# Kernel optimization log

Hardware: AMD Instinct MI355X
Metric: run time of the kernel (lower is better)

The kernel has to match this reference:

```python
import jax, jax.numpy as jnp
import numpy as np

D = 1024   # model dim (hard-coded in ClsNet)
H = 16     # num_heads
HD = D // H
FF = 2048  # torch TransformerEncoderLayer default dim_feedforward
B, LX, LY = 8, 512, 512
EPS = 1e-5
NEG = -1e9


def setup_inputs() -> dict:
    key = jax.random.key(0)
    ks = jax.random.split(key, 16)
    s = 0.02
    inp = {
        "x": jax.random.normal(ks[0], (B, LX, D), jnp.float32),
        "y": jax.random.normal(ks[1], (B, LY, D), jnp.float32),
        "cls": jax.random.normal(ks[2], (D,), jnp.float32) * s,
        "sep": jax.random.normal(ks[3], (D,), jnp.float32) * s,
        "px": jax.random.normal(ks[4], (D,), jnp.float32) * s,
        "py": jax.random.normal(ks[5], (D,), jnp.float32) * s,
        "Wqkv": jax.random.normal(ks[6], (3 * D, D), jnp.float32) * s,
        "bqkv": jnp.zeros((3 * D,), jnp.float32),
        "Wo": jax.random.normal(ks[7], (D, D), jnp.float32) * s,
        "bo": jnp.zeros((D,), jnp.float32),
        "W1": jax.random.normal(ks[8], (FF, D), jnp.float32) * s,
        "b1": jnp.zeros((FF,), jnp.float32),
        "W2": jax.random.normal(ks[9], (D, FF), jnp.float32) * s,
        "b2": jnp.zeros((D,), jnp.float32),
        "ln1_g": jnp.ones((D,), jnp.float32),
        "ln1_b": jnp.zeros((D,), jnp.float32),
        "ln2_g": jnp.ones((D,), jnp.float32),
        "ln2_b": jnp.zeros((D,), jnp.float32),
        "x_len": jax.random.randint(ks[10], (B,), 1, LX + 1, jnp.int32),
        "y_len": jax.random.randint(ks[11], (B,), 1, LY + 1, jnp.int32),
    }
    return inp


def _merge(x, y, cls, sep, px, py, x_len, y_len):
    # Vectorized version of ClsNet.merge: [CLS] x_i+px ... [SEP] y_i+py ... [SEP] pad...
    Bn, Lx, Dd = x.shape
    Ly = y.shape[1]
    S = Lx + Ly + 3
    pos = jnp.arange(S)[None, :]            # [1,S]
    lx = x_len[:, None]                     # [B,1]
    ly = y_len[:, None]
    is_cls = pos == 0                       # [1,S]
    is_x = (pos >= 1) & (pos <= lx)         # [B,S]
    is_sep1 = pos == lx + 1
    is_y = (pos >= lx + 2) & (pos <= lx + ly + 1)
    is_sep2 = pos == lx + ly + 2
    xi = jnp.clip(pos - 1, 0, Lx - 1)       # [1,S]
    yi = jnp.clip(pos - lx - 2, 0, Ly - 1)  # [B,S]
    xg = jnp.take_along_axis(x, xi[:, :, None], axis=1)  # [B,S,D] (broadcast batch)
    yg = jnp.take_along_axis(y, yi[:, :, None], axis=1)  # [B,S,D]
    seq = (jnp.where(is_x[..., None], xg + px, 0.0)
           + jnp.where(is_y[..., None], yg + py, 0.0)
           + is_cls[..., None] * cls
           + (is_sep1 | is_sep2)[..., None] * sep)       # [B,S,D]
    mask = is_cls | is_x | is_sep1 | is_y | is_sep2      # [B,S] True = valid token
    return seq, mask


def _ln(h, g, b):
    m = jnp.mean(h, axis=-1, keepdims=True)
    v = jnp.mean(jnp.square(h - m), axis=-1, keepdims=True)
    return (h - m) * jax.lax.rsqrt(v + EPS) * g + b


def _encoder_layer(seq, mask, Wqkv, bqkv, Wo, bo, W1, b1, W2, b2, ln1_g, ln1_b, ln2_g, ln2_b):
    Bn, S, Dd = seq.shape
    qkv = seq @ Wqkv.T + bqkv                              # [B,S,3D]
    q, k, v = jnp.split(qkv, 3, axis=-1)
    q = q.reshape(Bn, S, H, HD)
    k = k.reshape(Bn, S, H, HD)
    v = v.reshape(Bn, S, H, HD)
    bias = jnp.where(mask, 0.0, NEG)[:, None, None, :]     # padded KEYS masked out
    scores = jnp.einsum("bqhd,bkhd->bhqk", q, k) / np.sqrt(HD) + bias
    attn = jax.nn.softmax(scores, axis=-1)
    o = jnp.einsum("bhqk,bkhd->bqhd", attn, v).reshape(Bn, S, Dd)
    o = o @ Wo.T + bo
    h = _ln(seq + o, ln1_g, ln1_b)                          # post-norm (torch default)
    f = jax.nn.relu(h @ W1.T + b1) @ W2.T + b2
    return _ln(h + f, ln2_g, ln2_b)


def reference(x, y, cls, sep, px, py, Wqkv, bqkv, Wo, bo, W1, b1, W2, b2,
              ln1_g, ln1_b, ln2_g, ln2_b, x_len, y_len):
    seq, mask = _merge(x, y, cls, sep, px, py, x_len, y_len)
    out = _encoder_layer(seq, mask, Wqkv, bqkv, Wo, bo, W1, b1, W2, b2,
                         ln1_g, ln1_b, ln2_g, ln2_b)
    # torch code returns a[0] of the seq-first tensor -> the CLS position for all batches
    return out[:, 0, :]
```

## Files before the change

### kernel.cpp

```cpp
#include <hip/hip_runtime.h>
#include <hip/hip_bf16.h>

#define D_ 1024
#define H_ 16
#define FF_ 2048
#define B_ 8
#define S_ 1027
#define BS_ 8216
#define MPAD_ 8320
#define PSTR_ 1056
#define EPS_ 1e-5f
#define MAXGRID_ 512
#define NTILE_ 130

#define OFF_SEQ  0
#define OFF_RTHI 17039360
#define OFF_RTLO 17072128
#define OFF_S    17104896
#define OFF_P    17637376
#define OFF_CBAR 17907712
#define OFF_O0   20004864
#define OFF_ATT  20037632
#define OFF_F1   20070400
#define OFF_F2   20103168
#define OFF_BAR  20135936
#define OFF_Q0S  20140032
#define OFF_H0   20144128

typedef __hip_bfloat16 bf16;
typedef unsigned short u16;
typedef unsigned int u32;
typedef __attribute__((ext_vector_type(4))) float floatx4;
typedef __bf16 bf16x8 __attribute__((ext_vector_type(8)));

__device__ __forceinline__ float2 bfpair(u32 u) {
  union { u32 u; float f; } lo, hi;
  lo.u = u << 16; hi.u = u & 0xffff0000u;
  return make_float2(lo.f, hi.f);
}

__device__ __forceinline__ u32 f2bfbits(float f) {
  union { bf16 h; u16 u; } cv; cv.h = __float2bfloat16(f); return (u32)cv.u;
}

__device__ __forceinline__ void st_wt_f32(float* p, float v) {
  asm volatile("global_store_dword %0, %1, off sc0 sc1" :: "v"(p), "v"(v) : "memory");
}
__device__ __forceinline__ void st_wt_u16(u16* p, u32 v) {
  asm volatile("global_store_short %0, %1, off sc0 sc1" :: "v"(p), "v"(v) : "memory");
}
__device__ __forceinline__ void st_wt_v2(void* p, uint2 v) {
  asm volatile("global_store_dwordx2 %0, %1, off sc0 sc1" :: "v"(p), "v"(v) : "memory");
}
__device__ __forceinline__ void st_wt_f4(void* p, floatx4 v) {
  asm volatile("global_store_dwordx4 %0, %1, off sc0 sc1" :: "v"(p), "v"(v) : "memory");
}

__device__ __forceinline__ float blk_sum(float x, float* red) {
#pragma unroll
  for (int off = 32; off > 0; off >>= 1) x += __shfl_down(x, off, 64);
  __syncthreads();
  if ((threadIdx.x & 63) == 0) red[threadIdx.x >> 6] = x;
  __syncthreads();
  return red[0] + red[1] + red[2] + red[3];
}

__device__ __forceinline__ float blk_max(float x, float* red) {
#pragma unroll
  for (int off = 32; off > 0; off >>= 1) x = fmaxf(x, __shfl_down(x, off, 64));
  __syncthreads();
  if ((threadIdx.x & 63) == 0) red[threadIdx.x >> 6] = x;
  __syncthreads();
  return fmaxf(fmaxf(red[0], red[1]), fmaxf(red[2], red[3]));
}

__device__ __forceinline__ void gridbar(u32* bar, u32 phase) {
  asm volatile("s_waitcnt vmcnt(0) lgkmcnt(0)" ::: "memory");
  __syncthreads();
  if (threadIdx.x == 0) {
    __hip_atomic_fetch_add(bar + (blockIdx.x & 7) * 16, 1u,
                           __ATOMIC_RELAXED, __HIP_MEMORY_SCOPE_AGENT);
    const u32 target = (u32)gridDim.x * phase;
    int spins = 0;
    for (;;) {
      u32 s = 0;
#pragma unroll
      for (int i = 0; i < 8; ++i)
        s += __hip_atomic_load(bar + i * 16, __ATOMIC_RELAXED,
                               __HIP_MEMORY_SCOPE_AGENT);
      if (s >= target) break;
      __builtin_amdgcn_s_sleep(2);
      if (++spins > 400000) break;
    }
  }
  __syncthreads();
}

struct KP {
  const float *x, *y, *cls, *sep, *px, *py;
  const float *Wqkv, *bqkv, *Wo, *bo, *W1, *b1, *W2, *b2;
  const float *g1, *be1, *g2, *be2;
  const int *xl, *yl;
  bf16* seq; u16* RT_hi; u16* RT_lo; float* S; u16* P;
  float* cbar; float* o0; float* att; bf16* f1; float* f2; float* out;
  u32* bar;
};

__device__ __forceinline__ const float* row_src(const KP& p, int m,
                                                const int* lx8, const int* ly8,
                                                const float** add) {
  const int b = m / S_;
  const int s = m - b * S_;
  const int lx = lx8[b], ly = ly8[b];
  *add = nullptr;
  if (s == 0) return p.cls;
  if (s <= lx) { *add = p.px; return p.x + ((size_t)b * 512 + (s - 1)) * D_; }
  if (s == lx + 1) return p.sep;
  if (s <= lx + ly + 1) { *add = p.py; return p.y + ((size_t)b * 512 + (s - lx - 2)) * D_; }
  if (s == lx + ly + 2) return p.sep;
  return nullptr;
}

__global__ void __launch_bounds__(256, 2) mega_kernel(KP p) {
  __shared__ __align__(16) char smem_[33792];
  const int t = threadIdx.x;
  const int bid = blockIdx.x;
  const int G = gridDim.x;

  if (t == 0) __builtin_amdgcn_fence(__ATOMIC_ACQUIRE, "agent");
  __syncthreads();

  if (bid < 64) {
    const int h = bid >> 2, cc = bid & 3;
    float* cl = (float*)smem_;
    float* qs = (float*)(smem_ + 4096);
    *(float4*)&cl[t * 4] = ((const float4*)p.cls)[t];
    __syncthreads();
    const int r = t >> 2, j = t & 3;
    const float* wr = p.Wqkv + (size_t)(h * 64 + r) * D_;
    float acc = 0.f;
#pragma unroll 8
    for (int i = 0; i < 64; ++i) {
      float4 wv = *(const float4*)(wr + i * 16 + j * 4);
      const float* c4 = &cl[i * 16 + j * 4];
      acc += wv.x * c4[0] + wv.y * c4[1] + wv.z * c4[2] + wv.w * c4[3];
    }
    acc += __shfl_xor(acc, 1, 64);
    acc += __shfl_xor(acc, 2, 64);
    if (j == 0) qs[r] = (acc + p.bqkv[h * 64 + r]) * 0.125f;
    __syncthreads();
    const int c = cc * 256 + t;
    const float* Wk = p.Wqkv + (size_t)(D_ + h * 64) * D_ + c;
    float a2 = 0.f;
#pragma unroll 8
    for (int e = 0; e < 64; ++e) a2 += Wk[(size_t)e * D_] * qs[e];
    const u32 hb = f2bfbits(a2);
    union { u32 u; float f; } hv; hv.u = hb << 16;
    st_wt_u16(p.RT_hi + h * D_ + c, hb);
    st_wt_u16(p.RT_lo + h * D_ + c, f2bfbits(a2 - hv.f));
  } else {
    int lx8[8], ly8[8];
#pragma unroll
    for (int b = 0; b < 8; ++b) { lx8[b] = p.xl[b]; ly8[b] = p.yl[b]; }
    const int stride = G - 64;
    for (int m0 = bid - 64; m0 < BS_; m0 += 2 * stride) {
      const int m1 = m0 + stride;
      const float *ad0, *ad1 = nullptr;
      const float* s0 = row_src(p, m0, lx8, ly8, &ad0);
      const float* s1 = (m1 < BS_) ? row_src(p, m1, lx8, ly8, &ad1) : nullptr;
      float4 v0, a0v, v1, a1v;
      if (s0) v0 = ((const float4*)s0)[t];
      if (ad0) a0v = ((const float4*)ad0)[t];
      if (s1) v1 = ((const float4*)s1)[t];
      if (ad1) a1v = ((const float4*)ad1)[t];
      if (s0) {
        if (ad0) { v0.x += a0v.x; v0.y += a0v.y; v0.z += a0v.z; v0.w += a0v.w; }
        uint2 o;
        o.x = f2bfbits(v0.x) | (f2bfbits(v0.y) << 16);
        o.y = f2bfbits(v0.z) | (f2bfbits(v0.w) << 16);
        st_wt_v2((u16*)p.seq + (size_t)m0 * D_ + t * 4, o);
      }
      if (s1) {
        if (ad1) { v1.x += a1v.x; v1.y += a1v.y; v1.z += a1v.z; v1.w += a1v.w; }
        uint2 o;
        o.x = f2bfbits(v1.x) | (f2bfbits(v1.y) << 16);
        o.y = f2bfbits(v1.z) | (f2bfbits(v1.w) << 16);
        st_wt_v2((u16*)p.seq + (size_t)m1 * D_ + t * 4, o);
      }
    }
  }
  gridbar(p.bar, 1);

  for (int wk = bid; wk < NTILE_; wk += G) {
    const int m0 = wk * 64;
    bool valid = false;
#pragma unroll
    for (int b = 0; b < B_; ++b) {
      int rs = b * S_, re = rs + p.xl[b] + p.yl[b] + 3;
      if (m0 < re && m0 + 64 > rs) valid = true;
    }
    if (!valid) continue;
    const int w = t >> 6, lane = t & 63, lane16 = lane & 15, quad = lane >> 4;
    const int row = m0 + w * 16 + lane16;
    const u16* arow = (const u16*)p.seq + (size_t)row * D_ + quad * 8;
    const u16* bh = p.RT_hi + lane16 * D_ + quad * 8;
    const u16* bl = p.RT_lo + lane16 * D_ + quad * 8;
    floatx4 acc = {};
#pragma unroll 4
    for (int kt = 0; kt < 32; ++kt) {
      bf16x8 a  = *(const bf16x8*)(arow + kt * 32);
      bf16x8 vh = *(const bf16x8*)(bh + kt * 32);
      bf16x8 vl = *(const bf16x8*)(bl + kt * 32);
      acc = __builtin_amdgcn_mfma_f32_16x16x32_bf16(a, vh, acc, 0, 0, 0);
      acc = __builtin_amdgcn_mfma_f32_16x16x32_bf16(a, vl, acc, 0, 0, 0);
    }
    st_wt_f4(&p.S[(size_t)lane16 * MPAD_ + m0 + w * 16 + quad * 4], acc);
  }
  gridbar(p.bar, 2);

  {
    floatx4 z = {};
    for (int idx = bid * 256 + t; idx < 32768; idx += G * 256)
      st_wt_f4(p.cbar + (size_t)idx * 4, z);
  }
  for (int wk = bid; wk < 128; wk += G) {
    const int h = wk >> 3, b = wk & 7;
    const int n = p.xl[b] + p.yl[b] + 3;
    float* sc = (float*)smem_;
    float* red = (float*)(smem_ + PSTR_ * 4);
    const float* Sp = p.S + (size_t)h * MPAD_ + b * S_;
    float lmax = -3.0e38f;
    for (int k = t; k < n; k += 256) {
      float s = Sp[k];
      sc[k] = s;
      lmax = fmaxf(lmax, s);
    }
    const float gmax = blk_max(lmax, red);
    float lsum = 0.f;
    for (int k = t; k < n; k += 256) {
      float pr = __expf(sc[k] - gmax);
      sc[k] = pr;
      lsum += pr;
    }
    const float inv = 1.0f / blk_sum(lsum, red);
    u16* Pp = p.P + (size_t)(h * 8 + b) * PSTR_;
    for (int k = t; k < PSTR_; k += 256)
      st_wt_u16(Pp + k, (k < n) ? f2bfbits(sc[k] * inv) : 0u);
    __syncthreads();
  }
  gridbar(p.bar, 3);

  for (int wk = bid; wk < 512; wk += G) {
    const int ct = wk & 15, b = (wk >> 4) & 7, piece = wk >> 7;
    const int c0 = ct * 64;
    const int n = p.xl[b] + p.yl[b] + 3;
    const int nkt = (n + 31) >> 5;
    const int KR0[4] = {0, 9, 17, 25};
    const int KR1[4] = {9, 17, 25, 33};
    const int kt0 = KR0[piece];
    const int kt1 = nkt < KR1[piece] ? nkt : KR1[piece];
    u16* tile = (u16*)smem_;
    const int w = t >> 6, lane = t & 63, lane16 = lane & 15, quad = lane >> 4;
    const int sk = t >> 3, scg = (t & 7) * 8;
    floatx4 acc = {};
    uint4 v = make_uint4(0u, 0u, 0u, 0u);
    if (kt0 < kt1 && kt0 * 32 + sk < n)
      v = *(const uint4*)((const u16*)p.seq + (size_t)((size_t)b * S_ + kt0 * 32 + sk) * D_ + c0 + scg);
    bool any = (kt0 < kt1);
    for (int kt = kt0; kt < kt1; ++kt) {
      u16* tb = tile + (kt & 1) * (32 * 68);
      *(uint2*)&tb[sk * 68 + scg]     = make_uint2(v.x, v.y);
      *(uint2*)&tb[sk * 68 + scg + 4] = make_uint2(v.z, v.w);
      v = make_uint4(0u, 0u, 0u, 0u);
      if (kt + 1 < kt1 && (kt + 1) * 32 + sk < n)
        v = *(const uint4*)((const u16*)p.seq + (size_t)((size_t)b * S_ + (kt + 1) * 32 + sk) * D_ + c0 + scg);
      __syncthreads();
      bf16x8 a = *(const bf16x8*)(p.P + (size_t)(lane16 * 8 + b) * PSTR_ + kt * 32 + quad * 8);
      union { bf16x8 v8; u16 u[8]; } bu;
#pragma unroll
      for (int j = 0; j < 8; ++j)
        bu.u[j] = tb[(quad * 8 + j) * 68 + w * 16 + lane16];
      acc = __builtin_amdgcn_mfma_f32_16x16x32_bf16(a, bu.v8, acc, 0, 0, 0);
    }
    if (any) {
#pragma unroll
      for (int r = 0; r < 4; ++r)
        atomicAdd(&p.cbar[(size_t)(b * 16 + quad * 4 + r) * D_ + c0 + w * 16 + lane16], acc[r]);
    }
    __syncthreads();
  }
  gridbar(p.bar, 4);

  for (int wk = bid; wk < 256; wk += G) {
    float* lsf = (float*)smem_;
    const int hoff = ((wk * 4) >> 6) * D_;
#pragma unroll
    for (int i = 0; i < 8; ++i) {
      int flat = (t + i * 256) * 4;
      int b = flat >> 10, k = flat & 1023;
      *(float4*)&lsf[flat] = *(const float4*)(p.cbar + (size_t)b * 16384 + hoff + k);
    }
    __syncthreads();
    const int w = t >> 6, l = t & 63;
    const int r = wk * 4 + w;
    const float* W = p.Wqkv + (size_t)2048 * 1024;
    float acc[8] = {};
#pragma unroll
    for (int ch = 0; ch < 4; ++ch) {
      float4 wv = *(const float4*)(W + (size_t)r * D_ + ch * 256 + l * 4);
#pragma unroll
      for (int b = 0; b < 8; ++b) {
        const float* pp = &lsf[b * D_ + ch * 256 + l * 4];
        acc[b] += wv.x * pp[0] + wv.y * pp[1] + wv.z * pp[2] + wv.w * pp[3];
      }
    }
#pragma unroll
    for (int off = 32; off > 0; off >>= 1)
#pragma unroll
      for (int b = 0; b < 8; ++b) acc[b] += __shfl_down(acc[b], off, 64);
    if (l == 0) {
      const float bs = p.bqkv[2048 + r];
#pragma unroll
      for (int b = 0; b < 8; ++b) st_wt_f32(&p.o0[(size_t)b * D_ + r], acc[b] + bs);
    }
    __syncthreads();
  }
  gridbar(p.bar, 5);

  for (int wk = bid; wk < 256; wk += G) {
    float* lsf = (float*)smem_;
#pragma unroll
    for (int i = 0; i < 8; ++i) {
      int flat = (t + i * 256) * 4;
      *(float4*)&lsf[flat] = *(const float4*)(p.o0 + flat);
    }
    __syncthreads();
    const int w = t >> 6, l = t & 63;
    const int r = wk * 4 + w;
    float acc[8] = {};
#pragma unroll
    for (int ch = 0; ch < 4; ++ch) {
      float4 wv = *(const float4*)(p.Wo + (size_t)r * D_ + ch * 256 + l * 4);
#pragma unroll
      for (int b = 0; b < 8; ++b) {
        const float* pp = &lsf[b * D_ + ch * 256 + l * 4];
        acc[b] += wv.x * pp[0] + wv.y * pp[1] + wv.z * pp[2] + wv.w * pp[3];
      }
    }
#pragma unroll
    for (int off = 32; off > 0; off >>= 1)
#pragma unroll
      for (int b = 0; b < 8; ++b) acc[b] += __shfl_down(acc[b], off, 64);
    if (l == 0) {
      const float bs = p.bo[r];
#pragma unroll
      for (int b = 0; b < 8; ++b) st_wt_f32(&p.att[(size_t)b * D_ + r], acc[b] + bs);
    }
    __syncthreads();
  }
  gridbar(p.bar, 6);

  for (int wk = bid; wk < 512; wk += G) {
    float* lsf = (float*)smem_;
#pragma unroll
    for (int i = 0; i < 8; ++i) {
      int flat = (t + i * 256) * 4;
      int b = flat >> 10, k = flat & 1023;
      float4 av = *(const float4*)(p.att + (size_t)b * D_ + k);
      float4 cv = *(const float4*)(p.cls + k);
      av.x += cv.x; av.y += cv.y; av.z += cv.z; av.w += cv.w;
      *(float4*)&lsf[flat] = av;
    }
    __syncthreads();
    const int w = t >> 6, l = t & 63;
#pragma unroll
    for (int bb = 2 * w; bb < 2 * w + 2; ++bb) {
      float s = 0.f;
#pragma unroll
      for (int kk = 0; kk < 16; ++kk) s += lsf[bb * 1024 + kk * 64 + l];
#pragma unroll
      for (int off = 32; off > 0; off >>= 1) s += __shfl_xor(s, off, 64);
      const float mean = s * (1.f / D_);
      float vv = 0.f;
#pragma unroll
      for (int kk = 0; kk < 16; ++kk) {
        float d = lsf[bb * 1024 + kk * 64 + l] - mean; vv += d * d;
      }
#pragma unroll
      for (int off = 32; off > 0; off >>= 1) vv += __shfl_xor(vv, off, 64);
      const float rs = rsqrtf(vv * (1.f / D_) + EPS_);
#pragma unroll
      for (int kk = 0; kk < 16; ++kk) {
        int idx = kk * 64 + l;
        lsf[bb * 1024 + idx] =
            (lsf[bb * 1024 + idx] - mean) * rs * p.g1[idx] + p.be1[idx];
      }
    }
    __syncthreads();
    const int r = wk * 4 + w;
    float acc[8] = {};
#pragma unroll
    for (int ch = 0; ch < 4; ++ch) {
      float4 wv = *(const float4*)(p.W1 + (size_t)r * D_ + ch * 256 + l * 4);
#pragma unroll
      for (int b = 0; b < 8; ++b) {
        const float* pp = &lsf[b * D_ + ch * 256 + l * 4];
        acc[b] += wv.x * pp[0] + wv.y * pp[1] + wv.z * pp[2] + wv.w * pp[3];
      }
    }
#pragma unroll
    for (int off = 32; off > 0; off >>= 1)
#pragma unroll
      for (int b = 0; b < 8; ++b) acc[b] += __shfl_down(acc[b], off, 64);
    if (l == 0) {
      const float bs = p.b1[r];
#pragma unroll
      for (int b = 0; b < 8; ++b)
        st_wt_u16((u16*)p.f1 + (size_t)b * FF_ + r, f2bfbits(fmaxf(acc[b] + bs, 0.f)));
    }
    __syncthreads();
  }
  gridbar(p.bar, 7);

  for (int wk = bid; wk < 256; wk += G) {
    u16* lsb = (u16*)smem_;
#pragma unroll
    for (int i = 0; i < 8; ++i) {
      int flat = (t + i * 256) * 8;
      *(uint4*)&lsb[flat] = *(const uint4*)((const u16*)p.f1 + flat);
    }
    __syncthreads();
    const int w = t >> 6, l = t & 63;
    const int r = wk * 4 + w;
    float acc[8] = {};
#pragma unroll
    for (int ch = 0; ch < 8; ++ch) {
      float4 wv = *(const float4*)(p.W2 + (size_t)r * FF_ + ch * 256 + l * 4);
#pragma unroll
      for (int b = 0; b < 8; ++b) {
        uint2 u = *(const uint2*)&lsb[b * FF_ + ch * 256 + l * 4];
        float2 p0 = bfpair(u.x), p1 = bfpair(u.y);
        acc[b] += wv.x * p0.x + wv.y * p0.y + wv.z * p1.x + wv.w * p1.y;
      }
    }
#pragma unroll
    for (int off = 32; off > 0; off >>= 1)
#pragma unroll
      for (int b = 0; b < 8; ++b) acc[b] += __shfl_down(acc[b], off, 64);
    if (l == 0) {
      const float bs = p.b2[r];
#pragma unroll
      for (int b = 0; b < 8; ++b) st_wt_f32(&p.f2[(size_t)b * D_ + r], acc[b] + bs);
    }
    __syncthreads();
  }
  gridbar(p.bar, 8);

  for (int wk = bid; wk < 8; wk += G) {
    float* v = (float*)smem_;
    float* red = (float*)(smem_ + D_ * 4);
    for (int i = t; i < D_; i += 256) v[i] = p.cls[i] + p.att[wk * D_ + i];
    __syncthreads();
    float ls = 0.f;
    for (int i = t; i < D_; i += 256) ls += v[i];
    const float mean1 = blk_sum(ls, red) * (1.f / D_);
    float lv = 0.f;
    for (int i = t; i < D_; i += 256) { float dk = v[i] - mean1; lv += dk * dk; }
    const float var1 = blk_sum(lv, red) * (1.f / D_);
    const float rs1 = rsqrtf(var1 + EPS_);
    for (int i = t; i < D_; i += 256) {
      float h0v = (v[i] - mean1) * rs1 * p.g1[i] + p.be1[i];
      v[i] = h0v + p.f2[wk * D_ + i];
    }
    __syncthreads();
    float ls2 = 0.f;
    for (int i = t; i < D_; i += 256) ls2 += v[i];
    const float mean2 = blk_sum(ls2, red) * (1.f / D_);
    float lv2 = 0.f;
    for (int i = t; i < D_; i += 256) { float dk = v[i] - mean2; lv2 += dk * dk; }
    const float var2 = blk_sum(lv2, red) * (1.f / D_);
    const float rs2 = rsqrtf(var2 + EPS_);
    for (int i = t; i < D_; i += 256)
      p.out[wk * D_ + i] = (v[i] - mean2) * rs2 * p.g2[i] + p.be2[i];
    __syncthreads();
  }
}

__device__ __forceinline__ float block_sum(float x, float* red) {
  const int t = threadIdx.x;
  __syncthreads();
  red[t] = x;
  __syncthreads();
  for (int s = 128; s > 0; s >>= 1) {
    if (t < s) red[t] += red[t + s];
    __syncthreads();
  }
  return red[0];
}

__device__ __forceinline__ float block_max(float x, float* red) {
  const int t = threadIdx.x;
  __syncthreads();
  red[t] = x;
  __syncthreads();
  for (int s = 128; s > 0; s >>= 1) {
    if (t < s) red[t] = fmaxf(red[t], red[t + s]);
    __syncthreads();
  }
  return red[0];
}

__global__ void __launch_bounds__(256) build_seq_kernel(
    const float* __restrict__ x, const float* __restrict__ y,
    const float* __restrict__ cls, const float* __restrict__ sep,
    const float* __restrict__ px, const float* __restrict__ py,
    const int* __restrict__ x_len, const int* __restrict__ y_len,
    bf16* __restrict__ seq) {
  const int m = blockIdx.x, t = threadIdx.x;
  const int b = m / S_;
  const int s = m - b * S_;
  if (b >= B_) return;
  const float* src = nullptr;
  const float* add = nullptr;
  const int lx = x_len[b], ly = y_len[b];
  if (s == 0) src = cls;
  else if (s <= lx) { src = x + ((size_t)b * 512 + (s - 1)) * D_; add = px; }
  else if (s == lx + 1) src = sep;
  else if (s <= lx + ly + 1) { src = y + ((size_t)b * 512 + (s - lx - 2)) * D_; add = py; }
  else if (s == lx + ly + 2) src = sep;
  if (!src) return;
  float4 sv = ((const float4*)src)[t];
  if (add) {
    float4 av = ((const float4*)add)[t];
    sv.x += av.x; sv.y += av.y; sv.z += av.z; sv.w += av.w;
  }
  uint2 o;
  o.x = f2bfbits(sv.x) | (f2bfbits(sv.y) << 16);
  o.y = f2bfbits(sv.z) | (f2bfbits(sv.w) << 16);
  ((uint2*)(seq + (size_t)m * D_))[t] = o;
}

__global__ void __launch_bounds__(256) qproj_kernel(
    const float* __restrict__ cls, const float* __restrict__ Wqkv,
    const float* __restrict__ bqkv, float* __restrict__ q0s) {
  __shared__ float cl[D_];
  const int t = threadIdx.x;
  *(float4*)&cl[t * 4] = ((const float4*)cls)[t];
  __syncthreads();
  const int w = t >> 6, l = t & 63;
  const int r = blockIdx.x * 4 + w;
  float acc = 0.f;
#pragma unroll
  for (int ch = 0; ch < 4; ++ch) {
    float4 wv = *(const float4*)(Wqkv + (size_t)r * D_ + ch * 256 + l * 4);
    const float* c4 = &cl[ch * 256 + l * 4];
    acc += wv.x * c4[0] + wv.y * c4[1] + wv.z * c4[2] + wv.w * c4[3];
  }
#pragma unroll
  for (int off = 32; off > 0; off >>= 1) acc += __shfl_down(acc, off, 64);
  if (l == 0) q0s[r] = (acc + bqkv[r]) * 0.125f;
}

__global__ void __launch_bounds__(256) rproj_kernel(
    const float* __restrict__ Wqkv, const float* __restrict__ q0s,
    u16* __restrict__ RT_hi, u16* __restrict__ RT_lo) {
  const int h = blockIdx.y, cc = blockIdx.x, t = threadIdx.x;
  __shared__ float qs[64];
  if (t < 64) qs[t] = q0s[h * 64 + t];
  __syncthreads();
  const int c = cc * 256 + t;
  const float* Wk = Wqkv + (size_t)(D_ + h * 64) * D_ + c;
  float acc = 0.f;
#pragma unroll 8
  for (int e = 0; e < 64; ++e) acc += Wk[(size_t)e * D_] * qs[e];
  const u32 hb = f2bfbits(acc);
  union { u32 u; float f; } hv; hv.u = hb << 16;
  RT_hi[h * D_ + c] = (u16)hb;
  RT_lo[h * D_ + c] = (u16)f2bfbits(acc - hv.f);
}

__global__ void __launch_bounds__(256) scores_kernel(
    const bf16* __restrict__ seq, const u16* __restrict__ RT_hi,
    const u16* __restrict__ RT_lo, const int* __restrict__ x_len,
    const int* __restrict__ y_len, float* __restrict__ S) {
  const int m0 = blockIdx.x * 64;
  bool valid = false;
#pragma unroll
  for (int b = 0; b < B_; ++b) {
    int rs = b * S_, re = rs + x_len[b] + y_len[b] + 3;
    if (m0 < re && m0 + 64 > rs) valid = true;
  }
  if (!valid) return;
  const int t = threadIdx.x;
  const int w = t >> 6, lane = t & 63, lane16 = lane & 15, quad = lane >> 4;
  const int row = m0 + w * 16 + lane16;
  const u16* arow = (const u16*)seq + (size_t)row * D_ + quad * 8;
  const u16* bh = RT_hi + lane16 * D_ + quad * 8;
  const u16* bl = RT_lo + lane16 * D_ + quad * 8;
  floatx4 acc = {};
#pragma unroll 4
  for (int kt = 0; kt < 32; ++kt) {
    bf16x8 a  = *(const bf16x8*)(arow + kt * 32);
    bf16x8 vh = *(const bf16x8*)(bh + kt * 32);
    bf16x8 vl = *(const bf16x8*)(bl + kt * 32);
    acc = __builtin_amdgcn_mfma_f32_16x16x32_bf16(a, vh, acc, 0, 0, 0);
    acc = __builtin_amdgcn_mfma_f32_16x16x32_bf16(a, vl, acc, 0, 0, 0);
  }
  *(floatx4*)&S[(size_t)lane16 * MPAD_ + m0 + w * 16 + quad * 4] = acc;
}

__global__ void __launch_bounds__(256) softmax_kernel(
    const float* __restrict__ S, const int* __restrict__ x_len,
    const int* __restrict__ y_len, u16* __restrict__ P) {
  const int h = blockIdx.x, b = blockIdx.y, t = threadIdx.x;
  const int n = x_len[b] + y_len[b] + 3;
  __shared__ float sc[PSTR_];
  __shared__ float red[256];
  const float* Sp = S + (size_t)h * MPAD_ + b * S_;
  float lmax = -3.0e38f;
  for (int k = t; k < n; k += 256) {
    float s = Sp[k];
    sc[k] = s;
    lmax = fmaxf(lmax, s);
  }
  const float gmax = block_max(lmax, red);
  float lsum = 0.f;
  for (int k = t; k < n; k += 256) {
    float p = __expf(sc[k] - gmax);
    sc[k] = p;
    lsum += p;
  }
  const float inv = 1.0f / block_sum(lsum, red);
  u16* Pp = P + (size_t)(h * 8 + b) * PSTR_;
  for (int k = t; k < PSTR_; k += 256)
    Pp[k] = (k < n) ? (u16)f2bfbits(sc[k] * inv) : (u16)0;
}

__global__ void __launch_bounds__(256) cbar_kernel(
    const bf16* __restrict__ seq, const u16* __restrict__ P,
    const int* __restrict__ x_len, const int* __restrict__ y_len,
    float* __restrict__ cbar) {
  const int ct = blockIdx.x, b = blockIdx.y, t = threadIdx.x;
  const int c0 = ct * 64;
  const int n = x_len[b] + y_len[b] + 3;
  const int nkt = (n + 31) >> 5;
  __shared__ u16 tile[32 * 68];
  const int w = t >> 6, lane = t & 63, lane16 = lane & 15, quad = lane >> 4;
  const int sk = t >> 3, scg = (t & 7) * 8;
  floatx4 acc = {};
  for (int kt = 0; kt < nkt; ++kt) {
    const int k0 = kt * 32;
    __syncthreads();
    uint4 v = make_uint4(0u, 0u, 0u, 0u);
    if (k0 + sk < n)
      v = *(const uint4*)((const u16*)seq + (size_t)(b * S_ + k0 + sk) * D_ + c0 + scg);
    *(uint2*)&tile[sk * 68 + scg]     = make_uint2(v.x, v.y);
    *(uint2*)&tile[sk * 68 + scg + 4] = make_uint2(v.z, v.w);
    __syncthreads();
    bf16x8 a = *(const bf16x8*)(P + (size_t)(lane16 * 8 + b) * PSTR_ + k0 + quad * 8);
    union { bf16x8 v; u16 u[8]; } bu;
#pragma unroll
    for (int j = 0; j < 8; ++j)
      bu.u[j] = tile[(quad * 8 + j) * 68 + w * 16 + lane16];
    acc = __builtin_amdgcn_mfma_f32_16x16x32_bf16(a, bu.v, acc, 0, 0, 0);
  }
#pragma unroll
  for (int r = 0; r < 4; ++r)
    cbar[(size_t)(b * 16 + quad * 4 + r) * D_ + c0 + w * 16 + lane16] = acc[r];
}

template <int K, int N, int BSTR, bool INBF, bool OUTBF, bool RELU, bool PERHEAD>
__global__ void __launch_bounds__(256) gemv8_kernel(
    const void* __restrict__ in_, const float* __restrict__ W,
    const float* __restrict__ bias, void* __restrict__ out_) {
  const int t = threadIdx.x;
  const int hoff = PERHEAD ? ((blockIdx.x * 4) >> 6) * D_ : 0;
  __shared__ u16 lsb[INBF ? 8 * K : 1];
  __shared__ float lsf[INBF ? 1 : 8 * K];
  if (INBF) {
    const u16* in = (const u16*)in_;
    const int per = 8 * K / (256 * 8);
#pragma unroll
    for (int i = 0; i < per; ++i) {
      int flat = (t + i * 256) * 8;
      int b = flat / K, k = flat % K;
      *(uint4*)&lsb[flat] = *(const uint4*)(in + (size_t)b * BSTR + hoff + k);
    }
  } else {
    const float* in = (const float*)in_;
    const int per = 8 * K / (256 * 4);
#pragma unroll
    for (int i = 0; i < per; ++i) {
      int flat = (t + i * 256) * 4;
      int b = flat / K, k = flat % K;
      *(float4*)&lsf[flat] = *(const float4*)(in + (size_t)b * BSTR + hoff + k);
    }
  }
  __syncthreads();
  const int w = t >> 6, l = t & 63;
  const int r = blockIdx.x * 4 + w;
  float acc[8] = {};
#pragma unroll
  for (int ch = 0; ch < K / 256; ++ch) {
    float4 wv = *(const float4*)(W + (size_t)r * K + ch * 256 + l * 4);
#pragma unroll
    for (int b = 0; b < 8; ++b) {
      float i0, i1, i2, i3;
      if (INBF) {
        uint2 u = *(const uint2*)&lsb[b * K + ch * 256 + l * 4];
        float2 p0 = bfpair(u.x), p1 = bfpair(u.y);
        i0 = p0.x; i1 = p0.y; i2 = p1.x; i3 = p1.y;
      } else {
        const float* p = &lsf[b * K + ch * 256 + l * 4];
        i0 = p[0]; i1 = p[1]; i2 = p[2]; i3 = p[3];
      }
      acc[b] += wv.x * i0 + wv.y * i1 + wv.z * i2 + wv.w * i3;
    }
  }
#pragma unroll
  for (int off = 32; off > 0; off >>= 1)
#pragma unroll
    for (int b = 0; b < 8; ++b) acc[b] += __shfl_down(acc[b], off, 64);
  if (l == 0) {
    const float bs = bias[r];
#pragma unroll
    for (int b = 0; b < 8; ++b) {
      float v = acc[b] + bs;
      if (RELU) v = fmaxf(v, 0.f);
      if (OUTBF) ((bf16*)out_)[(size_t)b * N + r] = __float2bfloat16(v);
      else       ((float*)out_)[(size_t)b * N + r] = v;
    }
  }
}

template <bool SECOND>
__global__ void __launch_bounds__(256) ln_kernel(
    const float* __restrict__ cls, const float* __restrict__ a,
    const float* __restrict__ bvec, const float* __restrict__ g,
    const float* __restrict__ be, float* __restrict__ out) {
  const int b = blockIdx.x, t = threadIdx.x;
  __shared__ float v[D_];
  __shared__ float red[256];
  for (int i = t; i < D_; i += 256) {
    float val;
    if (SECOND) val = a[b * D_ + i] + bvec[b * D_ + i];
    else        val = cls[i] + a[b * D_ + i];
    v[i] = val;
  }
  __syncthreads();
  float ls = 0.f;
  for (int i = t; i < D_; i += 256) ls += v[i];
  const float mean = block_sum(ls, red) * (1.f / D_);
  float lv = 0.f;
  for (int i = t; i < D_; i += 256) { float dk = v[i] - mean; lv += dk * dk; }
  const float var = block_sum(lv, red) * (1.f / D_);
  const float rs = rsqrtf(var + EPS_);
  for (int i = t; i < D_; i += 256)
    out[b * D_ + i] = (v[i] - mean) * rs * g[i] + be[i];
}

extern "C" void kernel_launch(void* const* d_in, const int* in_sizes, int n_in,
                              void* d_out, int out_size, void* d_ws, size_t ws_size,
                              hipStream_t stream) {
  (void)in_sizes; (void)n_in; (void)out_size; (void)ws_size;
  const float* x    = (const float*)d_in[0];
  const float* y    = (const float*)d_in[1];
  const float* cls  = (const float*)d_in[2];
  const float* sep  = (const float*)d_in[3];
  const float* px   = (const float*)d_in[4];
  const float* py   = (const float*)d_in[5];
  const float* Wqkv = (const float*)d_in[6];
  const float* bqkv = (const float*)d_in[7];
  const float* Wo   = (const float*)d_in[8];
  const float* bo   = (const float*)d_in[9];
  const float* W1   = (const float*)d_in[10];
  const float* b1   = (const float*)d_in[11];
  const float* W2   = (const float*)d_in[12];
  const float* b2   = (const float*)d_in[13];
  const float* g1   = (const float*)d_in[14];
  const float* be1  = (const float*)d_in[15];
  const float* g2   = (const float*)d_in[16];
  const float* be2  = (const float*)d_in[17];
  const int* xl     = (const int*)d_in[18];
  const int* yl     = (const int*)d_in[19];

  char* ws = (char*)d_ws;
  bf16*  seq   = (bf16*)(ws + OFF_SEQ);
  u16*   RT_hi = (u16*)(ws + OFF_RTHI);
  u16*   RT_lo = (u16*)(ws + OFF_RTLO);
  float* S     = (float*)(ws + OFF_S);
  u16*   P     = (u16*)(ws + OFF_P);
  float* cbar  = (float*)(ws + OFF_CBAR);
  float* o0    = (float*)(ws + OFF_O0);
  float* att   = (float*)(ws + OFF_ATT);
  bf16*  f1    = (bf16*)(ws + OFF_F1);
  float* f2    = (float*)(ws + OFF_F2);
  u32*   bar   = (u32*)(ws + OFF_BAR);
  float* q0s   = (float*)(ws + OFF_Q0S);
  float* h0    = (float*)(ws + OFF_H0);

  KP kp;
  kp.x = x; kp.y = y; kp.cls = cls; kp.sep = sep; kp.px = px; kp.py = py;
  kp.Wqkv = Wqkv; kp.bqkv = bqkv; kp.Wo = Wo; kp.bo = bo;
  kp.W1 = W1; kp.b1 = b1; kp.W2 = W2; kp.b2 = b2;
  kp.g1 = g1; kp.be1 = be1; kp.g2 = g2; kp.be2 = be2;
  kp.xl = xl; kp.yl = yl;
  kp.seq = seq; kp.RT_hi = RT_hi; kp.RT_lo = RT_lo;
  kp.S = S; kp.P = P; kp.cbar = cbar;
  kp.o0 = o0; kp.att = att; kp.f1 = f1; kp.f2 = f2;
  kp.out = (float*)d_out;
  kp.bar = bar;

  static int mega_grid = -2;
  if (mega_grid == -2) {
    int nb = 0, ncu = 256;
    hipDeviceProp_t props;
    if (hipGetDeviceProperties(&props, 0) == hipSuccess)
      ncu = props.multiProcessorCount;
    if (hipOccupancyMaxActiveBlocksPerMultiprocessor(&nb, mega_kernel, 256, 0) ==
            hipSuccess && nb > 0) {
      long g = (long)nb * ncu;
      mega_grid = (int)(g < MAXGRID_ ? g : MAXGRID_);
    } else {
      mega_grid = -1;
    }
    if (mega_grid < 72) mega_grid = -1;
  }

  if (mega_grid > 0) {
    hipMemsetAsync(ws + OFF_BAR, 0, 4096, stream);
    mega_kernel<<<mega_grid, 256, 0, stream>>>(kp);
  } else {
    build_seq_kernel<<<MPAD_, 256, 0, stream>>>(x, y, cls, sep, px, py, xl, yl, seq);
    qproj_kernel<<<256, 256, 0, stream>>>(cls, Wqkv, bqkv, q0s);
    rproj_kernel<<<dim3(4, 16), 256, 0, stream>>>(Wqkv, q0s, RT_hi, RT_lo);
    scores_kernel<<<130, 256, 0, stream>>>(seq, RT_hi, RT_lo, xl, yl, S);
    softmax_kernel<<<dim3(16, 8), 256, 0, stream>>>(S, xl, yl, P);
    cbar_kernel<<<dim3(16, 8), 256, 0, stream>>>(seq, P, xl, yl, cbar);
    gemv8_kernel<1024, 1024, 16384, false, false, false, true>
        <<<256, 256, 0, stream>>>(cbar, Wqkv + (size_t)2048 * 1024, bqkv + 2048, o0);
    gemv8_kernel<1024, 1024, 1024, false, false, false, false>
        <<<256, 256, 0, stream>>>(o0, Wo, bo, att);
    ln_kernel<false><<<B_, 256, 0, stream>>>(cls, att, nullptr, g1, be1, h0);
    gemv8_kernel<1024, 2048, 1024, false, true, true, false>
        <<<512, 256, 0, stream>>>(h0, W1, b1, f1);
    gemv8_kernel<2048, 1024, 2048, true, false, false, false>
        <<<256, 256, 0, stream>>>(f1, W2, b2, f2);
    ln_kernel<true><<<B_, 256, 0, stream>>>(nullptr, h0, f2, g2, be2, (float*)d_out);
  }
}
```

Before: 224.7 us.

## Replace atomic cbar accumulation with per-piece partials and use generation-flag grid barrier

The cbar phase now writes each K-range piece's partial result to its own buffer with plain stores, and the following gemv phase sums the four partials on load. This removes the separate zeroing pass and the float atomicAdds into cbar. The grid barrier is also reworked: arrivals spread over 32 buckets, only block 0 polls the counters, and it then publishes a generation flag that the other blocks spin on, cutting polling traffic on the counters. The cost is four times the cbar memory traffic in the reduction phase, plus an extra hop through the flag on every barrier.

```diff
diff --git a/kernel.cpp b/kernel.cpp
--- a/kernel.cpp
+++ b/kernel.cpp
@@ -12,6 +12,7 @@
 #define EPS_ 1e-5f
 #define MAXGRID_ 512
 #define NTILE_ 130
+#define NBUCK_ 32
 
 #define OFF_SEQ  0
 #define OFF_RTHI 17039360
@@ -78,19 +79,30 @@
   asm volatile("s_waitcnt vmcnt(0) lgkmcnt(0)" ::: "memory");
   __syncthreads();
   if (threadIdx.x == 0) {
-    __hip_atomic_fetch_add(bar + (blockIdx.x & 7) * 16, 1u,
+    __hip_atomic_fetch_add(bar + (blockIdx.x & (NBUCK_ - 1)) * 16, 1u,
                            __ATOMIC_RELAXED, __HIP_MEMORY_SCOPE_AGENT);
-    const u32 target = (u32)gridDim.x * phase;
-    int spins = 0;
-    for (;;) {
-      u32 s = 0;
-#pragma unroll
-      for (int i = 0; i < 8; ++i)
-        s += __hip_atomic_load(bar + i * 16, __ATOMIC_RELAXED,
-                               __HIP_MEMORY_SCOPE_AGENT);
-      if (s >= target) break;
-      __builtin_amdgcn_s_sleep(2);
-      if (++spins > 400000) break;
+    u32* gen = bar + NBUCK_ * 16;
+    if (blockIdx.x == 0) {
+      const u32 target = (u32)gridDim.x * phase;
+      int spins = 0;
+      for (;;) {
+        u32 s = 0;
+#pragma unroll
+        for (int i = 0; i < NBUCK_; ++i)
+          s += __hip_atomic_load(bar + i * 16, __ATOMIC_RELAXED,
+                                 __HIP_MEMORY_SCOPE_AGENT);
+        if (s == target) break;
+        __builtin_amdgcn_s_sleep(1);
+        if (++spins > 300000) break;
+      }
+      __hip_atomic_store(gen, phase, __ATOMIC_RELAXED, __HIP_MEMORY_SCOPE_AGENT);
+    } else {
+      int spins = 0;
+      while (__hip_atomic_load(gen, __ATOMIC_RELAXED,
+                               __HIP_MEMORY_SCOPE_AGENT) < phase) {
+        __builtin_amdgcn_s_sleep(2);
+        if (++spins > 300000) break;
+      }
     }
   }
   __syncthreads();
@@ -102,7 +114,7 @@
   const float *g1, *be1, *g2, *be2;
   const int *xl, *yl;
   bf16* seq; u16* RT_hi; u16* RT_lo; float* S; u16* P;
-  float* cbar; float* o0; float* att; bf16* f1; float* f2; float* out;
+  float* cbar4; float* o0; float* att; bf16* f1; float* f2; float* out;
   u32* bar;
 };
 
@@ -218,11 +230,6 @@
   }
   gridbar(p.bar, 2);
 
-  {
-    floatx4 z = {};
-    for (int idx = bid * 256 + t; idx < 32768; idx += G * 256)
-      st_wt_f4(p.cbar + (size_t)idx * 4, z);
-  }
   for (int wk = bid; wk < 128; wk += G) {
     const int h = wk >> 3, b = wk & 7;
     const int n = p.xl[b] + p.yl[b] + 3;
@@ -266,7 +273,6 @@
     uint4 v = make_uint4(0u, 0u, 0u, 0u);
     if (kt0 < kt1 && kt0 * 32 + sk < n)
       v = *(const uint4*)((const u16*)p.seq + (size_t)((size_t)b * S_ + kt0 * 32 + sk) * D_ + c0 + scg);
-    bool any = (kt0 < kt1);
     for (int kt = kt0; kt < kt1; ++kt) {
       u16* tb = tile + (kt & 1) * (32 * 68);
       *(uint2*)&tb[sk * 68 + scg]     = make_uint2(v.x, v.y);
@@ -282,11 +288,10 @@
         bu.u[j] = tb[(quad * 8 + j) * 68 + w * 16 + lane16];
       acc = __builtin_amdgcn_mfma_f32_16x16x32_bf16(a, bu.v8, acc, 0, 0, 0);
     }
-    if (any) {
-#pragma unroll
-      for (int r = 0; r < 4; ++r)
-        atomicAdd(&p.cbar[(size_t)(b * 16 + quad * 4 + r) * D_ + c0 + w * 16 + lane16], acc[r]);
-    }
+    float* dst = p.cbar4 + (size_t)piece * 131072;
+#pragma unroll
+    for (int r = 0; r < 4; ++r)
+      st_wt_f32(&dst[(size_t)(b * 16 + quad * 4 + r) * D_ + c0 + w * 16 + lane16], acc[r]);
     __syncthreads();
   }
   gridbar(p.bar, 4);
@@ -298,7 +303,14 @@
     for (int i = 0; i < 8; ++i) {
       int flat = (t + i * 256) * 4;
       int b = flat >> 10, k = flat & 1023;
-      *(float4*)&lsf[flat] = *(const float4*)(p.cbar + (size_t)b * 16384 + hoff + k);
+      size_t off = (size_t)b * 16384 + hoff + k;
+      float4 a0 = *(const float4*)(p.cbar4 + off);
+      float4 a1 = *(const float4*)(p.cbar4 + 131072 + off);
+      float4 a2 = *(const float4*)(p.cbar4 + 262144 + off);
+      float4 a3 = *(const float4*)(p.cbar4 + 393216 + off);
+      a0.x += a1.x + a2.x + a3.x; a0.y += a1.y + a2.y + a3.y;
+      a0.z += a1.z + a2.z + a3.z; a0.w += a1.w + a2.w + a3.w;
+      *(float4*)&lsf[flat] = a0;
     }
     __syncthreads();
     const int w = t >> 6, l = t & 63;
@@ -790,7 +802,7 @@
   u16*   RT_lo = (u16*)(ws + OFF_RTLO);
   float* S     = (float*)(ws + OFF_S);
   u16*   P     = (u16*)(ws + OFF_P);
-  float* cbar  = (float*)(ws + OFF_CBAR);
+  float* cbar4 = (float*)(ws + OFF_CBAR);
   float* o0    = (float*)(ws + OFF_O0);
   float* att   = (float*)(ws + OFF_ATT);
   bf16*  f1    = (bf16*)(ws + OFF_F1);
@@ -806,7 +818,7 @@
   kp.g1 = g1; kp.be1 = be1; kp.g2 = g2; kp.be2 = be2;
   kp.xl = xl; kp.yl = yl;
   kp.seq = seq; kp.RT_hi = RT_hi; kp.RT_lo = RT_lo;
-  kp.S = S; kp.P = P; kp.cbar = cbar;
+  kp.S = S; kp.P = P; kp.cbar4 = cbar4;
   kp.o0 = o0; kp.att = att; kp.f1 = f1; kp.f2 = f2;
   kp.out = (float*)d_out;
   kp.bar = bar;
@@ -836,9 +848,9 @@
     rproj_kernel<<<dim3(4, 16), 256, 0, stream>>>(Wqkv, q0s, RT_hi, RT_lo);
     scores_kernel<<<130, 256, 0, stream>>>(seq, RT_hi, RT_lo, xl, yl, S);
     softmax_kernel<<<dim3(16, 8), 256, 0, stream>>>(S, xl, yl, P);
-    cbar_kernel<<<dim3(16, 8), 256, 0, stream>>>(seq, P, xl, yl, cbar);
+    cbar_kernel<<<dim3(16, 8), 256, 0, stream>>>(seq, P, xl, yl, cbar4);
     gemv8_kernel<1024, 1024, 16384, false, false, false, true>
-        <<<256, 256, 0, stream>>>(cbar, Wqkv + (size_t)2048 * 1024, bqkv + 2048, o0);
+        <<<256, 256, 0, stream>>>(cbar4, Wqkv + (size_t)2048 * 1024, bqkv + 2048, o0);
     gemv8_kernel<1024, 1024, 1024, false, false, false, false>
         <<<256, 256, 0, stream>>>(o0, Wo, bo, att);
     ln_kernel<false><<<B_, 256, 0, stream>>>(cls, att, nullptr, g1, be1, h0);
```

Result: faster. 204.7 us (-8.9%).
